# Kernel tuning notes

Hardware: AMD Instinct MI355X
Metric: run time of the kernel (lower is better)

## Reference

```python
import jax, jax.numpy as jnp
import numpy as np

DIM_LOC = 2
DIM_EMBED = 32
HID = 2 * DIM_EMBED  # 64, GRUCell input and hidden size
B, T = 65536, 24


def leaky(v):
    return jnp.where(v > 0, v, 0.2 * v)


def setup_inputs() -> dict:
    key = jax.random.key(0)
    ks = jax.random.split(key, 10)
    s = lambda fan: 1.0 / np.sqrt(fan)
    return {
        "x": jax.random.normal(ks[0], (B, T, DIM_LOC), dtype=jnp.float32),
        "W_loc": jax.random.uniform(ks[1], (DIM_LOC, DIM_EMBED), jnp.float32, -s(DIM_LOC), s(DIM_LOC)),
        "b_loc": jax.random.uniform(ks[2], (DIM_EMBED,), jnp.float32, -s(DIM_LOC), s(DIM_LOC)),
        "time_table": jax.random.normal(ks[3], (24, DIM_EMBED), dtype=jnp.float32),
        "W_ih": jax.random.uniform(ks[4], (3 * HID, HID), jnp.float32, -s(HID), s(HID)),
        "W_hh": jax.random.uniform(ks[5], (3 * HID, HID), jnp.float32, -s(HID), s(HID)),
        "b_ih": jax.random.uniform(ks[6], (3 * HID,), jnp.float32, -s(HID), s(HID)),
        "b_hh": jax.random.uniform(ks[7], (3 * HID,), jnp.float32, -s(HID), s(HID)),
        "W_pred": jax.random.uniform(ks[8], (HID, 1), jnp.float32, -s(HID), s(HID)),
        "b_pred": jax.random.uniform(ks[9], (1,), jnp.float32, -s(HID), s(HID)),
    }


def reference(x, W_loc, b_loc, time_table, W_ih, W_hh, b_ih, b_hh, W_pred, b_pred):
    Bn, Tn, _ = x.shape
    # location embedding + LeakyReLU(0.2): [B, T, 32]
    embed_x = leaky(jnp.einsum('btl,le->bte', x, W_loc) + b_loc)
    # time embedding + LeakyReLU(0.2) for t = 0..T-1: [T, 32]
    embed_t = leaky(time_table[:Tn])

    def gru_step(h, inp_t):
        ex_t, et_t = inp_t  # [B,32], [32]
        inp = jnp.concatenate(
            [ex_t, jnp.broadcast_to(et_t, (ex_t.shape[0], et_t.shape[0]))], axis=1)  # [B,64]
        gi = inp @ W_ih.T + b_ih   # [B, 192]
        gh = h @ W_hh.T + b_hh     # [B, 192]
        i_r, i_z, i_n = jnp.split(gi, 3, axis=1)
        h_r, h_z, h_n = jnp.split(gh, 3, axis=1)
        r = jax.nn.sigmoid(i_r + h_r)
        z = jax.nn.sigmoid(i_z + h_z)
        n = jnp.tanh(i_n + r * h_n)
        h_new = (1.0 - z) * n + z * h
        return h_new, None

    h0 = jnp.zeros((Bn, HID), dtype=x.dtype)
    xs = (jnp.transpose(embed_x, (1, 0, 2)), embed_t)  # time-major
    h_final, _ = jax.lax.scan(gru_step, h0, xs)
    out = jax.nn.sigmoid(h_final @ W_pred + b_pred)  # [B,1]
    return out.ravel()
```

## Files before the change

### kernel.cpp

```cpp
#include <hip/hip_runtime.h>
#include <hip/hip_bf16.h>

#define TN 24
#define HID 64
#define LOG2E 1.4426950408889634f

#define WS_GIC_F   0
#define WS_BHN_F   4608
#define WS_WLC_F   4672
#define WS_FRAG_B  19072

#define HHI_OFF  0
#define HLO_OFF  18432
#define WHH_OFF  36864
#define WI_OFF   61440
#define BHN_OFF  73728
#define WLC_OFF  73984
#define LDS_BYTES 74368

typedef __attribute__((ext_vector_type(8))) short bf16x8;
typedef __attribute__((ext_vector_type(4))) float f32x4;
typedef __attribute__((ext_vector_type(2))) float f32x2;

__device__ __forceinline__ ushort bf16rn(float f) {
    uint x = __float_as_uint(f);
    return (ushort)((x + 0x7fffu + ((x >> 16) & 1u)) >> 16);
}
__device__ __forceinline__ uint cvtpk_bf16(float lo, float hi) {
    uint r;
    asm("v_cvt_pk_bf16_f32 %0, %1, %2" : "=v"(r) : "v"(lo), "v"(hi));
    return r;
}
__device__ __forceinline__ float exp2p_(float x) {
    float r; asm("v_exp_f32 %0, %1" : "=v"(r) : "v"(x)); return r;
}
__device__ __forceinline__ float exp2n_(float x) {
    float r; asm("v_exp_f32 %0, -%1" : "=v"(r) : "v"(x)); return r;
}
__device__ __forceinline__ float sigm(float v) {
    return __builtin_amdgcn_rcpf(1.0f + __expf(-v));
}

extern "C" __global__ void __launch_bounds__(256)
traj_gru_pre(const float* __restrict__ Wloc, const float* __restrict__ bloc,
             const float* __restrict__ tt, const float* __restrict__ Wih,
             const float* __restrict__ Whh, const float* __restrict__ bih,
             const float* __restrict__ bhh, float* __restrict__ ws)
{
    const int b = blockIdx.x, tid = threadIdx.x;
    if (b < 36) {
        if (tid < 64) {
            const int er = tid & 15, cp = tid >> 4;
            const float* src;
            float s;
            if (b < 8) {
                int g = b >> 2, a = b & 3;
                src = Wih + (size_t)(g * 64 + a * 16 + er) * 64 + 8 * cp;
                s = LOG2E;
            } else if (b < 32) {
                int t = b - 8, g = t >> 3, r = t & 7, a = r >> 1, f = r & 1;
                src = Whh + (size_t)(g * 64 + a * 16 + er) * 64 + 32 * f + 8 * cp;
                s = (g == 2) ? 2.0f * LOG2E : LOG2E;
            } else {
                int a = b - 32;
                src = Wih + (size_t)(128 + a * 16 + er) * 64 + 8 * cp;
                s = 2.0f * LOG2E;
            }
            union { ushort u[8]; bf16x8 v; } fr;
            #pragma unroll
            for (int j = 0; j < 8; ++j) fr.u[j] = bf16rn(s * src[j]);
            *(bf16x8*)((char*)ws + WS_FRAG_B + ((size_t)b * 64 + tid) * 16) = fr.v;
        }
    } else if (b < 38) {
        const int base = (b - 36) * 2304;
        for (int i = tid; i < 2304; i += 256) {
            int idx = base + i, t = idx / 192, g = idx % 192;
            float acc = bih[g] + (g < 128 ? bhh[g] : 0.0f);
            const float* ttr = tt + t * 32;
            const float* wr  = Wih + g * 64 + 32;
            #pragma unroll
            for (int k = 0; k < 32; ++k) {
                float e = ttr[k];
                e = fmaxf(e, 0.2f * e);
                acc = fmaf(wr[k], e, acc);
            }
            ws[WS_GIC_F + idx] = acc * (g < 128 ? LOG2E : 2.0f * LOG2E);
        }
    } else {
        if (tid < 64) ws[WS_BHN_F + tid] = 2.0f * LOG2E * bhh[128 + tid];
        if (tid < 96) ws[WS_WLC_F + tid] = (tid < 64) ? Wloc[tid] : bloc[tid - 64];
    }
}

extern "C" __global__ void __launch_bounds__(512, 4)
traj_gru_mfma(const float* __restrict__ x, const float* __restrict__ ws,
              const float* __restrict__ Wpred, const float* __restrict__ bpred,
              float* __restrict__ out)
{
    extern __shared__ __align__(16) char L[];
    float*  Lf   = (float*)L;
    char*   whhS = L + WHH_OFF;
    char*   wiS  = L + WI_OFF;

    const int tid  = threadIdx.x;
    const int lane = tid & 63;
    const int wid  = tid >> 6;
    const int er   = lane & 15;
    const int cp   = lane >> 4;

    const char* fb = (const char*)ws + WS_FRAG_B;
    for (int i = tid; i < 36 * 64; i += 512) {
        int f = i >> 6, l = i & 63;
        bf16x8 v = *(const bf16x8*)(fb + (size_t)i * 16);
        char* dst;
        if (f < 8)       dst = wiS  + ((size_t)f * 64 + l) * 16;
        else if (f < 32) dst = whhS + ((size_t)(f - 8) * 64 + l) * 16;
        else             dst = wiS  + ((size_t)(f - 24) * 64 + l) * 16;
        *(bf16x8*)dst = v;
    }
    if (tid < 64) Lf[BHN_OFF / 4 + tid] = ws[WS_BHN_F + tid];
    if (tid < 96) Lf[WLC_OFF / 4 + tid] = ws[WS_WLC_F + tid];
    __syncthreads();

    const f32x2* wlc2 = (const f32x2*)(Lf + WLC_OFF / 4);
    ushort* Hhi = (ushort*)(L + HHI_OFF) + (size_t)(wid * 16) * 72;
    ushort* Hlo = (ushort*)(L + HLO_OFF) + (size_t)(wid * 16) * 72;

    const long long eg = (long long)(blockIdx.x * 8 + wid) * 16 + er;
    const float* xr = x + eg * (TN * 2);

    f32x2 hold2[4][2];
    #pragma unroll
    for (int a = 0; a < 4; ++a)
        #pragma unroll
        for (int p = 0; p < 2; ++p) hold2[a][p] = (f32x2){0.0f, 0.0f};

    const f32x2 one2    = {1.0f, 1.0f};
    const f32x2 negtwo2 = {-2.0f, -2.0f};

    float2 xv = *(const float2*)(xr);

    #pragma unroll 1
    for (int t = 0; t < TN; ++t) {
        const int tn = (t + 1 < TN) ? t + 1 : TN - 1;
        float2 xv_next = *(const float2*)(xr + tn * 2);

        union { uint u[4]; bf16x8 v; } exf;
        {
            f32x2 xx = {xv.x, xv.x}, yy = {xv.y, xv.y};
            #pragma unroll
            for (int jp = 0; jp < 4; ++jp) {
                int kp = 4 * cp + jp;
                f32x2 w1 = wlc2[kp], w2 = wlc2[16 + kp], bl = wlc2[32 + kp];
                f32x2 v = __builtin_elementwise_fma(xx, w1,
                          __builtin_elementwise_fma(yy, w2, bl));
                float v0 = fmaxf(v.x, 0.2f * v.x);
                float v1 = fmaxf(v.y, 0.2f * v.y);
                exf.u[jp] = cvtpk_bf16(v0, v1);
            }
        }

        const float* gt = ws + WS_GIC_F + t * 192;
        f32x4 accR[4], accZ[4], accNi[4], accNh[4];
        #pragma unroll
        for (int a = 0; a < 4; ++a) {
            accR[a]  = *(const f32x4*)(gt + a * 16 + 4 * cp);
            accZ[a]  = *(const f32x4*)(gt + 64 + a * 16 + 4 * cp);
            accNi[a] = *(const f32x4*)(gt + 128 + a * 16 + 4 * cp);
            accNh[a] = *(const f32x4*)(Lf + BHN_OFF / 4 + a * 16 + 4 * cp);
        }

        #pragma unroll
        for (int a = 0; a < 4; ++a) {
            bf16x8 wr = *(const bf16x8*)(wiS + ((size_t)a * 64 + lane) * 16);
            bf16x8 wz = *(const bf16x8*)(wiS + ((size_t)(4 + a) * 64 + lane) * 16);
            bf16x8 wn = *(const bf16x8*)(wiS + ((size_t)(8 + a) * 64 + lane) * 16);
            accR[a]  = __builtin_amdgcn_mfma_f32_16x16x32_bf16(wr, exf.v, accR[a], 0, 0, 0);
            accZ[a]  = __builtin_amdgcn_mfma_f32_16x16x32_bf16(wz, exf.v, accZ[a], 0, 0, 0);
            accNi[a] = __builtin_amdgcn_mfma_f32_16x16x32_bf16(wn, exf.v, accNi[a], 0, 0, 0);
        }

        if (t > 0) {
            bf16x8 hhi0 = *(const bf16x8*)&Hhi[er * 72 + 8 * cp];
            bf16x8 hhi1 = *(const bf16x8*)&Hhi[er * 72 + 32 + 8 * cp];
            bf16x8 hlo0 = *(const bf16x8*)&Hlo[er * 72 + 8 * cp];
            bf16x8 hlo1 = *(const bf16x8*)&Hlo[er * 72 + 32 + 8 * cp];
            #pragma unroll
            for (int a = 0; a < 4; ++a) {
                bf16x8 wr0 = *(const bf16x8*)(whhS + ((size_t)(a * 2 + 0) * 64 + lane) * 16);
                bf16x8 wr1 = *(const bf16x8*)(whhS + ((size_t)(a * 2 + 1) * 64 + lane) * 16);
                accR[a] = __builtin_amdgcn_mfma_f32_16x16x32_bf16(wr0, hhi0, accR[a], 0, 0, 0);
                accR[a] = __builtin_amdgcn_mfma_f32_16x16x32_bf16(wr1, hhi1, accR[a], 0, 0, 0);
                bf16x8 wz0 = *(const bf16x8*)(whhS + ((size_t)(8 + a * 2 + 0) * 64 + lane) * 16);
                bf16x8 wz1 = *(const bf16x8*)(whhS + ((size_t)(8 + a * 2 + 1) * 64 + lane) * 16);
                accZ[a] = __builtin_amdgcn_mfma_f32_16x16x32_bf16(wz0, hhi0, accZ[a], 0, 0, 0);
                accZ[a] = __builtin_amdgcn_mfma_f32_16x16x32_bf16(wz1, hhi1, accZ[a], 0, 0, 0);
                bf16x8 wn0 = *(const bf16x8*)(whhS + ((size_t)(16 + a * 2 + 0) * 64 + lane) * 16);
                bf16x8 wn1 = *(const bf16x8*)(whhS + ((size_t)(16 + a * 2 + 1) * 64 + lane) * 16);
                accNh[a] = __builtin_amdgcn_mfma_f32_16x16x32_bf16(wn0, hhi0, accNh[a], 0, 0, 0);
                accNh[a] = __builtin_amdgcn_mfma_f32_16x16x32_bf16(wn1, hhi1, accNh[a], 0, 0, 0);
                accNh[a] = __builtin_amdgcn_mfma_f32_16x16x32_bf16(wn0, hlo0, accNh[a], 0, 0, 0);
                accNh[a] = __builtin_amdgcn_mfma_f32_16x16x32_bf16(wn1, hlo1, accNh[a], 0, 0, 0);
            }
        }

        #pragma unroll
        for (int a = 0; a < 4; ++a) {
            uint hiw[2], low[2];
            #pragma unroll
            for (int p = 0; p < 2; ++p) {
                f32x2 aR  = {accR[a][2 * p],  accR[a][2 * p + 1]};
                f32x2 aZ  = {accZ[a][2 * p],  accZ[a][2 * p + 1]};
                f32x2 aNi = {accNi[a][2 * p], accNi[a][2 * p + 1]};
                f32x2 aNh = {accNh[a][2 * p], accNh[a][2 * p + 1]};
                f32x2 eR = {exp2n_(aR.x), exp2n_(aR.y)};
                f32x2 eZ = {exp2n_(aZ.x), exp2n_(aZ.y)};
                f32x2 dR = eR + one2;
                f32x2 dZ = eZ + one2;
                f32x2 r  = {__builtin_amdgcn_rcpf(dR.x), __builtin_amdgcn_rcpf(dR.y)};
                f32x2 z  = {__builtin_amdgcn_rcpf(dZ.x), __builtin_amdgcn_rcpf(dZ.y)};
                f32x2 np = __builtin_elementwise_fma(r, aNh, aNi);
                f32x2 e2 = {exp2p_(np.x), exp2p_(np.y)};
                f32x2 d2 = e2 + one2;
                f32x2 rc = {__builtin_amdgcn_rcpf(d2.x), __builtin_amdgcn_rcpf(d2.y)};
                f32x2 n  = __builtin_elementwise_fma(rc, negtwo2, one2);
                f32x2 hm = hold2[a][p] - n;
                f32x2 h  = __builtin_elementwise_fma(z, hm, n);
                hold2[a][p] = h;
                uint whi = cvtpk_bf16(h.x, h.y);
                f32x2 hh = {__uint_as_float(whi << 16), __uint_as_float(whi & 0xffff0000u)};
                f32x2 lo = h - hh;
                hiw[p] = whi;
                low[p] = cvtpk_bf16(lo.x, lo.y);
            }
            uint2 whiv = {hiw[0], hiw[1]};
            uint2 wlov = {low[0], low[1]};
            *(uint2*)&Hhi[er * 72 + 16 * a + 4 * cp] = whiv;
            *(uint2*)&Hlo[er * 72 + 16 * a + 4 * cp] = wlov;
        }

        xv = xv_next;
    }

    float part = 0.0f;
    #pragma unroll
    for (int a = 0; a < 4; ++a) {
        f32x4 wp = *(const f32x4*)(Wpred + 16 * a + 4 * cp);
        #pragma unroll
        for (int p = 0; p < 2; ++p) {
            part = fmaf(hold2[a][p].x, wp[2 * p], part);
            part = fmaf(hold2[a][p].y, wp[2 * p + 1], part);
        }
    }
    part += __shfl_xor(part, 16);
    part += __shfl_xor(part, 32);
    if (cp == 0) out[eg] = sigm(part + bpred[0]);
}

extern "C" void kernel_launch(void* const* d_in, const int* in_sizes, int n_in,
                              void* d_out, int out_size, void* d_ws, size_t ws_size,
                              hipStream_t stream) {
    const float* x     = (const float*)d_in[0];
    const float* Wloc  = (const float*)d_in[1];
    const float* bloc  = (const float*)d_in[2];
    const float* tt    = (const float*)d_in[3];
    const float* Wih   = (const float*)d_in[4];
    const float* Whh   = (const float*)d_in[5];
    const float* bih   = (const float*)d_in[6];
    const float* bhh   = (const float*)d_in[7];
    const float* Wpred = (const float*)d_in[8];
    const float* bpred = (const float*)d_in[9];
    float* out = (float*)d_out;
    float* ws  = (float*)d_ws;

    (void)hipFuncSetAttribute((const void*)traj_gru_mfma,
                              hipFuncAttributeMaxDynamicSharedMemorySize, LDS_BYTES);

    hipLaunchKernelGGL(traj_gru_pre, dim3(39), dim3(256), 0, stream,
                       Wloc, bloc, tt, Wih, Whh, bih, bhh, ws);
    hipLaunchKernelGGL(traj_gru_mfma, dim3(512), dim3(512), LDS_BYTES, stream,
                       x, ws, Wpred, bpred, out);
}
```

Measured before the change: 119.2 us.

## Process two 16-row batch fragments per wave to reuse weight fragments

Each wave now handles 32 sequences (two 16-row MFMA fragments) instead of 16, so every weight fragment loaded from LDS feeds two MFMAs. Grid is halved to 256 blocks, LDS per block grows to about 111 KB, and launch bounds drop to 2 blocks per CU. The n-gate hidden bias is kept in registers rather than reloaded every step. This trades fewer resident waves (256 blocks on 256 CUs, one block each) and higher register pressure for more independent MFMA work per wave and fewer LDS weight reads.

After: 114.2 us. 1.04x faster.

```diff
diff --git a/kernel.cpp b/kernel.cpp
--- a/kernel.cpp
+++ b/kernel.cpp
@@ -11,12 +11,12 @@
 #define WS_FRAG_B  19072
 
 #define HHI_OFF  0
-#define HLO_OFF  18432
-#define WHH_OFF  36864
-#define WI_OFF   61440
-#define BHN_OFF  73728
-#define WLC_OFF  73984
-#define LDS_BYTES 74368
+#define HLO_OFF  36864
+#define WHH_OFF  73728
+#define WI_OFF   98304
+#define BHN_OFF  110592
+#define WLC_OFF  110848
+#define LDS_BYTES 111232
 
 typedef __attribute__((ext_vector_type(8))) short bf16x8;
 typedef __attribute__((ext_vector_type(4))) float f32x4;
@@ -92,7 +92,7 @@
     }
 }
 
-extern "C" __global__ void __launch_bounds__(512, 4)
+extern "C" __global__ void __launch_bounds__(512, 2)
 traj_gru_mfma(const float* __restrict__ x, const float* __restrict__ ws,
               const float* __restrict__ Wpred, const float* __restrict__ bpred,
               float* __restrict__ out)
@@ -123,138 +123,183 @@
     __syncthreads();
 
     const f32x2* wlc2 = (const f32x2*)(Lf + WLC_OFF / 4);
-    ushort* Hhi = (ushort*)(L + HHI_OFF) + (size_t)(wid * 16) * 72;
-    ushort* Hlo = (ushort*)(L + HLO_OFF) + (size_t)(wid * 16) * 72;
-
-    const long long eg = (long long)(blockIdx.x * 8 + wid) * 16 + er;
-    const float* xr = x + eg * (TN * 2);
-
-    f32x2 hold2[4][2];
+    ushort* Hhi = (ushort*)(L + HHI_OFF) + (size_t)(wid * 32) * 72;
+    ushort* Hlo = (ushort*)(L + HLO_OFF) + (size_t)(wid * 32) * 72;
+
+    f32x4 bhnR[4];
     #pragma unroll
     for (int a = 0; a < 4; ++a)
-        #pragma unroll
-        for (int p = 0; p < 2; ++p) hold2[a][p] = (f32x2){0.0f, 0.0f};
+        bhnR[a] = *(const f32x4*)(Lf + BHN_OFF / 4 + a * 16 + 4 * cp);
+
+    const int ego = (blockIdx.x * 8 + wid) * 32;
+    const float* xr0 = x + (size_t)(ego + er) * (TN * 2);
+    const float* xr1 = x + (size_t)(ego + 16 + er) * (TN * 2);
+
+    f32x2 hold2[2][4][2];
+    #pragma unroll
+    for (int bf = 0; bf < 2; ++bf)
+        #pragma unroll
+        for (int a = 0; a < 4; ++a)
+            #pragma unroll
+            for (int p = 0; p < 2; ++p) hold2[bf][a][p] = (f32x2){0.0f, 0.0f};
 
     const f32x2 one2    = {1.0f, 1.0f};
     const f32x2 negtwo2 = {-2.0f, -2.0f};
 
-    float2 xv = *(const float2*)(xr);
+    float2 xv0 = *(const float2*)(xr0);
+    float2 xv1 = *(const float2*)(xr1);
 
     #pragma unroll 1
     for (int t = 0; t < TN; ++t) {
         const int tn = (t + 1 < TN) ? t + 1 : TN - 1;
-        float2 xv_next = *(const float2*)(xr + tn * 2);
-
-        union { uint u[4]; bf16x8 v; } exf;
+        float2 xv0n = *(const float2*)(xr0 + tn * 2);
+        float2 xv1n = *(const float2*)(xr1 + tn * 2);
+
+        union { uint u[4]; bf16x8 v; } exf0, exf1;
         {
-            f32x2 xx = {xv.x, xv.x}, yy = {xv.y, xv.y};
+            f32x2 xx0 = {xv0.x, xv0.x}, yy0 = {xv0.y, xv0.y};
+            f32x2 xx1 = {xv1.x, xv1.x}, yy1 = {xv1.y, xv1.y};
             #pragma unroll
             for (int jp = 0; jp < 4; ++jp) {
                 int kp = 4 * cp + jp;
                 f32x2 w1 = wlc2[kp], w2 = wlc2[16 + kp], bl = wlc2[32 + kp];
-                f32x2 v = __builtin_elementwise_fma(xx, w1,
-                          __builtin_elementwise_fma(yy, w2, bl));
-                float v0 = fmaxf(v.x, 0.2f * v.x);
-                float v1 = fmaxf(v.y, 0.2f * v.y);
-                exf.u[jp] = cvtpk_bf16(v0, v1);
+                f32x2 v0 = __builtin_elementwise_fma(xx0, w1,
+                           __builtin_elementwise_fma(yy0, w2, bl));
+                f32x2 v1 = __builtin_elementwise_fma(xx1, w1,
+                           __builtin_elementwise_fma(yy1, w2, bl));
+                exf0.u[jp] = cvtpk_bf16(fmaxf(v0.x, 0.2f * v0.x), fmaxf(v0.y, 0.2f * v0.y));
+                exf1.u[jp] = cvtpk_bf16(fmaxf(v1.x, 0.2f * v1.x), fmaxf(v1.y, 0.2f * v1.y));
             }
         }
 
         const float* gt = ws + WS_GIC_F + t * 192;
-        f32x4 accR[4], accZ[4], accNi[4], accNh[4];
+        f32x4 gR[4], gZ[4], gNi[4];
         #pragma unroll
         for (int a = 0; a < 4; ++a) {
-            accR[a]  = *(const f32x4*)(gt + a * 16 + 4 * cp);
-            accZ[a]  = *(const f32x4*)(gt + 64 + a * 16 + 4 * cp);
-            accNi[a] = *(const f32x4*)(gt + 128 + a * 16 + 4 * cp);
-            accNh[a] = *(const f32x4*)(Lf + BHN_OFF / 4 + a * 16 + 4 * cp);
-        }
+            gR[a]  = *(const f32x4*)(gt + a * 16 + 4 * cp);
+            gZ[a]  = *(const f32x4*)(gt + 64 + a * 16 + 4 * cp);
+            gNi[a] = *(const f32x4*)(gt + 128 + a * 16 + 4 * cp);
+        }
+
+        f32x4 accR[2][4], accZ[2][4], accNi[2][4], accNh[2][4];
 
         #pragma unroll
         for (int a = 0; a < 4; ++a) {
             bf16x8 wr = *(const bf16x8*)(wiS + ((size_t)a * 64 + lane) * 16);
             bf16x8 wz = *(const bf16x8*)(wiS + ((size_t)(4 + a) * 64 + lane) * 16);
             bf16x8 wn = *(const bf16x8*)(wiS + ((size_t)(8 + a) * 64 + lane) * 16);
-            accR[a]  = __builtin_amdgcn_mfma_f32_16x16x32_bf16(wr, exf.v, accR[a], 0, 0, 0);
-            accZ[a]  = __builtin_amdgcn_mfma_f32_16x16x32_bf16(wz, exf.v, accZ[a], 0, 0, 0);
-            accNi[a] = __builtin_amdgcn_mfma_f32_16x16x32_bf16(wn, exf.v, accNi[a], 0, 0, 0);
+            accR[0][a]  = __builtin_amdgcn_mfma_f32_16x16x32_bf16(wr, exf0.v, gR[a], 0, 0, 0);
+            accR[1][a]  = __builtin_amdgcn_mfma_f32_16x16x32_bf16(wr, exf1.v, gR[a], 0, 0, 0);
+            accZ[0][a]  = __builtin_amdgcn_mfma_f32_16x16x32_bf16(wz, exf0.v, gZ[a], 0, 0, 0);
+            accZ[1][a]  = __builtin_amdgcn_mfma_f32_16x16x32_bf16(wz, exf1.v, gZ[a], 0, 0, 0);
+            accNi[0][a] = __builtin_amdgcn_mfma_f32_16x16x32_bf16(wn, exf0.v, gNi[a], 0, 0, 0);
+            accNi[1][a] = __builtin_amdgcn_mfma_f32_16x16x32_bf16(wn, exf1.v, gNi[a], 0, 0, 0);
         }
 
         if (t > 0) {
-            bf16x8 hhi0 = *(const bf16x8*)&Hhi[er * 72 + 8 * cp];
-            bf16x8 hhi1 = *(const bf16x8*)&Hhi[er * 72 + 32 + 8 * cp];
-            bf16x8 hlo0 = *(const bf16x8*)&Hlo[er * 72 + 8 * cp];
-            bf16x8 hlo1 = *(const bf16x8*)&Hlo[er * 72 + 32 + 8 * cp];
+            bf16x8 hh0[2], hh1[2], hl0[2], hl1[2];
+            #pragma unroll
+            for (int bf = 0; bf < 2; ++bf) {
+                const int row = (bf * 16 + er) * 72;
+                hh0[bf] = *(const bf16x8*)&Hhi[row + 8 * cp];
+                hh1[bf] = *(const bf16x8*)&Hhi[row + 32 + 8 * cp];
+                hl0[bf] = *(const bf16x8*)&Hlo[row + 8 * cp];
+                hl1[bf] = *(const bf16x8*)&Hlo[row + 32 + 8 * cp];
+            }
             #pragma unroll
             for (int a = 0; a < 4; ++a) {
                 bf16x8 wr0 = *(const bf16x8*)(whhS + ((size_t)(a * 2 + 0) * 64 + lane) * 16);
                 bf16x8 wr1 = *(const bf16x8*)(whhS + ((size_t)(a * 2 + 1) * 64 + lane) * 16);
-                accR[a] = __builtin_amdgcn_mfma_f32_16x16x32_bf16(wr0, hhi0, accR[a], 0, 0, 0);
-                accR[a] = __builtin_amdgcn_mfma_f32_16x16x32_bf16(wr1, hhi1, accR[a], 0, 0, 0);
+                accR[0][a] = __builtin_amdgcn_mfma_f32_16x16x32_bf16(wr0, hh0[0], accR[0][a], 0, 0, 0);
+                accR[0][a] = __builtin_amdgcn_mfma_f32_16x16x32_bf16(wr1, hh1[0], accR[0][a], 0, 0, 0);
+                accR[1][a] = __builtin_amdgcn_mfma_f32_16x16x32_bf16(wr0, hh0[1], accR[1][a], 0, 0, 0);
+                accR[1][a] = __builtin_amdgcn_mfma_f32_16x16x32_bf16(wr1, hh1[1], accR[1][a], 0, 0, 0);
                 bf16x8 wz0 = *(const bf16x8*)(whhS + ((size_t)(8 + a * 2 + 0) * 64 + lane) * 16);
                 bf16x8 wz1 = *(const bf16x8*)(whhS + ((size_t)(8 + a * 2 + 1) * 64 + lane) * 16);
-                accZ[a] = __builtin_amdgcn_mfma_f32_16x16x32_bf16(wz0, hhi0, accZ[a], 0, 0, 0);
-                accZ[a] = __builtin_amdgcn_mfma_f32_16x16x32_bf16(wz1, hhi1, accZ[a], 0, 0, 0);
+                accZ[0][a] = __builtin_amdgcn_mfma_f32_16x16x32_bf16(wz0, hh0[0], accZ[0][a], 0, 0, 0);
+                accZ[0][a] = __builtin_amdgcn_mfma_f32_16x16x32_bf16(wz1, hh1[0], accZ[0][a], 0, 0, 0);
+                accZ[1][a] = __builtin_amdgcn_mfma_f32_16x16x32_bf16(wz0, hh0[1], accZ[1][a], 0, 0, 0);
+                accZ[1][a] = __builtin_amdgcn_mfma_f32_16x16x32_bf16(wz1, hh1[1], accZ[1][a], 0, 0, 0);
                 bf16x8 wn0 = *(const bf16x8*)(whhS + ((size_t)(16 + a * 2 + 0) * 64 + lane) * 16);
                 bf16x8 wn1 = *(const bf16x8*)(whhS + ((size_t)(16 + a * 2 + 1) * 64 + lane) * 16);
-                accNh[a] = __builtin_amdgcn_mfma_f32_16x16x32_bf16(wn0, hhi0, accNh[a], 0, 0, 0);
-                accNh[a] = __builtin_amdgcn_mfma_f32_16x16x32_bf16(wn1, hhi1, accNh[a], 0, 0, 0);
-                accNh[a] = __builtin_amdgcn_mfma_f32_16x16x32_bf16(wn0, hlo0, accNh[a], 0, 0, 0);
-                accNh[a] = __builtin_amdgcn_mfma_f32_16x16x32_bf16(wn1, hlo1, accNh[a], 0, 0, 0);
-            }
-        }
-
-        #pragma unroll
-        for (int a = 0; a < 4; ++a) {
-            uint hiw[2], low[2];
-            #pragma unroll
-            for (int p = 0; p < 2; ++p) {
-                f32x2 aR  = {accR[a][2 * p],  accR[a][2 * p + 1]};
-                f32x2 aZ  = {accZ[a][2 * p],  accZ[a][2 * p + 1]};
-                f32x2 aNi = {accNi[a][2 * p], accNi[a][2 * p + 1]};
-                f32x2 aNh = {accNh[a][2 * p], accNh[a][2 * p + 1]};
-                f32x2 eR = {exp2n_(aR.x), exp2n_(aR.y)};
-                f32x2 eZ = {exp2n_(aZ.x), exp2n_(aZ.y)};
-                f32x2 dR = eR + one2;
-                f32x2 dZ = eZ + one2;
-                f32x2 r  = {__builtin_amdgcn_rcpf(dR.x), __builtin_amdgcn_rcpf(dR.y)};
-                f32x2 z  = {__builtin_amdgcn_rcpf(dZ.x), __builtin_amdgcn_rcpf(dZ.y)};
-                f32x2 np = __builtin_elementwise_fma(r, aNh, aNi);
-                f32x2 e2 = {exp2p_(np.x), exp2p_(np.y)};
-                f32x2 d2 = e2 + one2;
-                f32x2 rc = {__builtin_amdgcn_rcpf(d2.x), __builtin_amdgcn_rcpf(d2.y)};
-                f32x2 n  = __builtin_elementwise_fma(rc, negtwo2, one2);
-                f32x2 hm = hold2[a][p] - n;
-                f32x2 h  = __builtin_elementwise_fma(z, hm, n);
-                hold2[a][p] = h;
-                uint whi = cvtpk_bf16(h.x, h.y);
-                f32x2 hh = {__uint_as_float(whi << 16), __uint_as_float(whi & 0xffff0000u)};
-                f32x2 lo = h - hh;
-                hiw[p] = whi;
-                low[p] = cvtpk_bf16(lo.x, lo.y);
-            }
-            uint2 whiv = {hiw[0], hiw[1]};
-            uint2 wlov = {low[0], low[1]};
-            *(uint2*)&Hhi[er * 72 + 16 * a + 4 * cp] = whiv;
-            *(uint2*)&Hlo[er * 72 + 16 * a + 4 * cp] = wlov;
-        }
-
-        xv = xv_next;
-    }
-
-    float part = 0.0f;
+                accNh[0][a] = __builtin_amdgcn_mfma_f32_16x16x32_bf16(wn0, hh0[0], bhnR[a], 0, 0, 0);
+                accNh[0][a] = __builtin_amdgcn_mfma_f32_16x16x32_bf16(wn1, hh1[0], accNh[0][a], 0, 0, 0);
+                accNh[0][a] = __builtin_amdgcn_mfma_f32_16x16x32_bf16(wn0, hl0[0], accNh[0][a], 0, 0, 0);
+                accNh[0][a] = __builtin_amdgcn_mfma_f32_16x16x32_bf16(wn1, hl1[0], accNh[0][a], 0, 0, 0);
+                accNh[1][a] = __builtin_amdgcn_mfma_f32_16x16x32_bf16(wn0, hh0[1], bhnR[a], 0, 0, 0);
+                accNh[1][a] = __builtin_amdgcn_mfma_f32_16x16x32_bf16(wn1, hh1[1], accNh[1][a], 0, 0, 0);
+                accNh[1][a] = __builtin_amdgcn_mfma_f32_16x16x32_bf16(wn0, hl0[1], accNh[1][a], 0, 0, 0);
+                accNh[1][a] = __builtin_amdgcn_mfma_f32_16x16x32_bf16(wn1, hl1[1], accNh[1][a], 0, 0, 0);
+            }
+        } else {
+            #pragma unroll
+            for (int bf = 0; bf < 2; ++bf)
+                #pragma unroll
+                for (int a = 0; a < 4; ++a) accNh[bf][a] = bhnR[a];
+        }
+
+        #pragma unroll
+        for (int bf = 0; bf < 2; ++bf) {
+            const int row = (bf * 16 + er) * 72;
+            #pragma unroll
+            for (int a = 0; a < 4; ++a) {
+                uint hiw[2], low[2];
+                #pragma unroll
+                for (int p = 0; p < 2; ++p) {
+                    f32x2 aR  = {accR[bf][a][2 * p],  accR[bf][a][2 * p + 1]};
+                    f32x2 aZ  = {accZ[bf][a][2 * p],  accZ[bf][a][2 * p + 1]};
+                    f32x2 aNi = {accNi[bf][a][2 * p], accNi[bf][a][2 * p + 1]};
+                    f32x2 aNh = {accNh[bf][a][2 * p], accNh[bf][a][2 * p + 1]};
+                    f32x2 eR = {exp2n_(aR.x), exp2n_(aR.y)};
+                    f32x2 eZ = {exp2n_(aZ.x), exp2n_(aZ.y)};
+                    f32x2 dR = eR + one2;
+                    f32x2 dZ = eZ + one2;
+                    f32x2 r  = {__builtin_amdgcn_rcpf(dR.x), __builtin_amdgcn_rcpf(dR.y)};
+                    f32x2 z  = {__builtin_amdgcn_rcpf(dZ.x), __builtin_amdgcn_rcpf(dZ.y)};
+                    f32x2 np = __builtin_elementwise_fma(r, aNh, aNi);
+                    f32x2 e2 = {exp2p_(np.x), exp2p_(np.y)};
+                    f32x2 d2 = e2 + one2;
+                    f32x2 rc = {__builtin_amdgcn_rcpf(d2.x), __builtin_amdgcn_rcpf(d2.y)};
+                    f32x2 n  = __builtin_elementwise_fma(rc, negtwo2, one2);
+                    f32x2 hm = hold2[bf][a][p] - n;
+                    f32x2 h  = __builtin_elementwise_fma(z, hm, n);
+                    hold2[bf][a][p] = h;
+                    uint whi = cvtpk_bf16(h.x, h.y);
+                    f32x2 hh = {__uint_as_float(whi << 16), __uint_as_float(whi & 0xffff0000u)};
+                    f32x2 lo = h - hh;
+                    hiw[p] = whi;
+                    low[p] = cvtpk_bf16(lo.x, lo.y);
+                }
+                uint2 whiv = {hiw[0], hiw[1]};
+                uint2 wlov = {low[0], low[1]};
+                *(uint2*)&Hhi[row + 16 * a + 4 * cp] = whiv;
+                *(uint2*)&Hlo[row + 16 * a + 4 * cp] = wlov;
+            }
+        }
+
+        xv0 = xv0n;
+        xv1 = xv1n;
+    }
+
+    float p0 = 0.0f, p1 = 0.0f;
     #pragma unroll
     for (int a = 0; a < 4; ++a) {
         f32x4 wp = *(const f32x4*)(Wpred + 16 * a + 4 * cp);
         #pragma unroll
         for (int p = 0; p < 2; ++p) {
-            part = fmaf(hold2[a][p].x, wp[2 * p], part);
-            part = fmaf(hold2[a][p].y, wp[2 * p + 1], part);
-        }
-    }
-    part += __shfl_xor(part, 16);
-    part += __shfl_xor(part, 32);
-    if (cp == 0) out[eg] = sigm(part + bpred[0]);
+            p0 = fmaf(hold2[0][a][p].x, wp[2 * p], p0);
+            p0 = fmaf(hold2[0][a][p].y, wp[2 * p + 1], p0);
+            p1 = fmaf(hold2[1][a][p].x, wp[2 * p], p1);
+            p1 = fmaf(hold2[1][a][p].y, wp[2 * p + 1], p1);
+        }
+    }
+    p0 += __shfl_xor(p0, 16);  p0 += __shfl_xor(p0, 32);
+    p1 += __shfl_xor(p1, 16);  p1 += __shfl_xor(p1, 32);
+    if (cp == 0) {
+        float bp = bpred[0];
+        out[ego + er]      = sigm(p0 + bp);
+        out[ego + 16 + er] = sigm(p1 + bp);
+    }
 }
 
 extern "C" void kernel_launch(void* const* d_in, const int* in_sizes, int n_in,
@@ -278,6 +323,6 @@
 
     hipLaunchKernelGGL(traj_gru_pre, dim3(39), dim3(256), 0, stream,
                        Wloc, bloc, tt, Wih, Whh, bih, bhh, ws);
-    hipLaunchKernelGGL(traj_gru_mfma, dim3(512), dim3(512), LDS_BYTES, stream,
+    hipLaunchKernelGGL(traj_gru_mfma, dim3(256), dim3(512), LDS_BYTES, stream,
                        x, ws, Wpred, bpred, out);
 }
```
